# Performance work log

Measured on AMD Instinct MI355X. Metric: run time of the kernel, lower is better.

The kernel has to match this reference:

```python
import jax, jax.numpy as jnp
import numpy as np

C = 256
NUM_HEADS = 8
HEAD_DIM = C // NUM_HEADS
EPS = 1e-5


def setup_inputs() -> dict:
    key = jax.random.key(0)
    ks = jax.random.split(key, 12)
    b, h, w = 8, 64, 64
    s = 1.0 / np.sqrt(C)
    return {
        "cortical": jax.random.normal(ks[0], (b, C, h, w), jnp.float32),
        "subcortical": jax.random.normal(ks[1], (b, C, h, w), jnp.float32),
        "ventricular": jax.random.normal(ks[2], (b, C, h, w), jnp.float32),
        "in_proj_w": jax.random.uniform(ks[3], (3 * C, C), jnp.float32, -s, s),
        "in_proj_b": jnp.zeros((3 * C,), jnp.float32),
        "out_proj_w": jax.random.uniform(ks[4], (C, C), jnp.float32, -s, s),
        "out_proj_b": jnp.zeros((C,), jnp.float32),
        "ln_gamma": jnp.ones((C,), jnp.float32),
        "ln_beta": jnp.zeros((C,), jnp.float32),
        "conv_w": jax.random.uniform(ks[5], (C, 3 * C), jnp.float32, -1.0 / np.sqrt(3 * C), 1.0 / np.sqrt(3 * C)),
        "conv_b": jnp.zeros((C,), jnp.float32),
    }


def _forward(cortical, subcortical, ventricular,
             in_proj_w, in_proj_b, out_proj_w, out_proj_b,
             ln_gamma, ln_beta, conv_w, conv_b):
    b, c, h, w = cortical.shape
    # stack regions -> tokens of seq_len 3: (b,h,w,3,c) -> (N,3,c)
    regions = jnp.stack([cortical, subcortical, ventricular], axis=1)  # (b,3,c,h,w)
    x = regions.transpose(0, 3, 4, 1, 2).reshape(b * h * w, 3, c)
    # fused QKV projection
    qkv = x @ in_proj_w.T + in_proj_b  # (N,3,3c)
    q, k, v = jnp.split(qkv, 3, axis=-1)
    # split heads: (N,3,H,D)
    def heads(t):
        return t.reshape(-1, 3, NUM_HEADS, HEAD_DIM)
    q, k, v = heads(q), heads(k), heads(v)
    scores = jnp.einsum("nshd,nthd->nhst", q, k) / np.sqrt(HEAD_DIM)
    attn = jax.nn.softmax(scores, axis=-1)
    o = jnp.einsum("nhst,nthd->nshd", attn, v).reshape(-1, 3, c)
    o = o @ out_proj_w.T + out_proj_b
    # residual + LayerNorm over channels
    y = o + x
    mu = y.mean(-1, keepdims=True)
    var = y.var(-1, keepdims=True)
    y = (y - mu) * jax.lax.rsqrt(var + EPS) * ln_gamma + ln_beta
    # (N,3,c) -> (b,h,w,3c) region-major == torch cat along channel dim
    fused = y.reshape(b, h, w, 3 * c)
    out = fused @ conv_w.T + conv_b  # 1x1 conv as matmul
    return out.transpose(0, 3, 1, 2)  # (b,c,h,w)


def reference(cortical, subcortical, ventricular, in_proj_w, in_proj_b,
              out_proj_w, out_proj_b, ln_gamma, ln_beta, conv_w, conv_b):
    return _forward(cortical, subcortical, ventricular, in_proj_w, in_proj_b,
                    out_proj_w, out_proj_b, ln_gamma, ln_beta, conv_w, conv_b)
```

## Files before the change

kernel.cpp:

```cpp
#include <hip/hip_runtime.h>

typedef __bf16 bf16x8 __attribute__((ext_vector_type(8)));
typedef float  f32x4  __attribute__((ext_vector_type(4)));

#define XOFF 0
#define OOFF 49152
#define OBUFSZ 7680
#define PSOFF 64512
#define PQOFF 66048
#define MUOFF 67584
#define RSOFF 67968
#define SMEM_BYTES 68352

static __device__ __forceinline__ unsigned short f2b(float f) {
  __bf16 h = (__bf16)f;
  return __builtin_bit_cast(unsigned short, h);
}

__global__ void convert_weights(const float* __restrict__ w_in,
                                const float* __restrict__ w_out,
                                const float* __restrict__ w_conv,
                                __bf16* __restrict__ ws) {
  int gid = blockIdx.x * 256 + threadIdx.x;
  int i4 = gid * 4;
  const float* src;
  int off;
  if (i4 < 196608)      { src = w_in;   off = i4; }
  else if (i4 < 262144) { src = w_out;  off = i4 - 196608; }
  else                  { src = w_conv; off = i4 - 262144; }
  float4 f = *(const float4*)(src + off);
  ws[i4 + 0] = (__bf16)f.x;
  ws[i4 + 1] = (__bf16)f.y;
  ws[i4 + 2] = (__bf16)f.z;
  ws[i4 + 3] = (__bf16)f.w;
}

__global__ __launch_bounds__(256, 2) void crf_fused(
    const float* __restrict__ cort,
    const float* __restrict__ subc,
    const float* __restrict__ vent,
    const __bf16* __restrict__ w_in,
    const float* __restrict__ b_in,
    const __bf16* __restrict__ w_out,
    const float* __restrict__ b_out,
    const float* __restrict__ gamma,
    const float* __restrict__ beta,
    const __bf16* __restrict__ w_conv,
    const float* __restrict__ b_conv,
    float* __restrict__ out) {
  extern __shared__ char smem[];
  const int tid  = threadIdx.x;
  const int lane = tid & 63;
  const int wv   = tid >> 6;
  const int l15  = lane & 15;
  const int l4   = lane >> 4;
  const int blk  = blockIdx.x;
  const int img  = blk >> 7;
  const int pixbase = (blk & 127) << 5;
  const size_t base = (size_t)img * (256 * 4096) + pixbase;

  {
    const float* rp0 = cort + base;
    const float* rp1 = subc + base;
    const float* rp2 = vent + base;
#pragma unroll
    for (int si = 0; si < 3; ++si) {
      const float* rp = (si == 0) ? rp0 : (si == 1) ? rp1 : rp2;
#pragma unroll
      for (int t = 0; t < 16; ++t) {
        int idx = t * 256 + tid;
        int p   = idx & 31;
        int c   = (idx >> 5) * 2;
        float f0 = rp[(size_t)c * 4096 + p];
        float f1 = rp[(size_t)(c + 1) * 4096 + p];
        int m = si * 32 + p;
        unsigned off = ((unsigned)(m * 512 + c * 2)) ^ ((unsigned)(m & 7) << 4);
        unsigned pack = (unsigned)f2b(f0) | ((unsigned)f2b(f1) << 16);
        *(unsigned*)(smem + XOFF + off) = pack;
      }
    }
  }

  f32x4 accY[6][4] = {};

  __syncthreads();

  const int ph = wv & 1;
  const int hg = wv >> 1;
  const float SC = 0.17677669529663687f;

  for (int hh = 0; hh < 4; ++hh) {
    const int h = hg * 4 + hh;
    f32x4 acc[3][6] = {};
#pragma unroll
    for (int ks = 0; ks < 8; ++ks) {
      const int k0 = ks * 32;
      bf16x8 af[3], bfr[6];
#pragma unroll
      for (int s = 0; s < 3; ++s) {
        int m = s * 32 + ph * 16 + l15;
        unsigned off = ((unsigned)(m * 512 + (k0 + l4 * 8) * 2)) ^ ((unsigned)(m & 7) << 4);
        af[s] = *(const bf16x8*)(smem + XOFF + off);
      }
#pragma unroll
      for (int j = 0; j < 6; ++j) {
        int jb = (j >> 1) * 256 + h * 32 + (j & 1) * 16 + l15;
        bfr[j] = *(const bf16x8*)(w_in + (size_t)jb * 256 + k0 + l4 * 8);
      }
#pragma unroll
      for (int s = 0; s < 3; ++s)
#pragma unroll
        for (int j = 0; j < 6; ++j)
          acc[s][j] = __builtin_amdgcn_mfma_f32_16x16x32_bf16(af[s], bfr[j], acc[s][j], 0, 0, 0);
    }
#pragma unroll
    for (int jq = 0; jq < 2; ++jq) {
      float bq = b_in[h * 32 + jq * 16 + l15];
      float bk = b_in[256 + h * 32 + jq * 16 + l15];
      float bv = b_in[512 + h * 32 + jq * 16 + l15];
#pragma unroll
      for (int s = 0; s < 3; ++s)
#pragma unroll
        for (int r = 0; r < 4; ++r) {
          acc[s][jq][r]     += bq;
          acc[s][2 + jq][r] += bk;
          acc[s][4 + jq][r] += bv;
        }
    }
    char* ob = smem + OOFF + hg * OBUFSZ;
#pragma unroll
    for (int si = 0; si < 3; ++si) {
      float pp[3][4];
#pragma unroll
      for (int ti = 0; ti < 3; ++ti)
#pragma unroll
        for (int r = 0; r < 4; ++r)
          pp[ti][r] = acc[si][0][r] * acc[ti][2][r] + acc[si][1][r] * acc[ti][3][r];
#pragma unroll
      for (int mask = 1; mask <= 8; mask <<= 1)
#pragma unroll
        for (int ti = 0; ti < 3; ++ti)
#pragma unroll
          for (int r = 0; r < 4; ++r)
            pp[ti][r] += __shfl_xor(pp[ti][r], mask);
#pragma unroll
      for (int r = 0; r < 4; ++r) {
        float s0 = pp[0][r] * SC, s1 = pp[1][r] * SC, s2 = pp[2][r] * SC;
        float mx = fmaxf(fmaxf(s0, s1), s2);
        float e0 = __expf(s0 - mx), e1 = __expf(s1 - mx), e2 = __expf(s2 - mx);
        float inv = 1.f / (e0 + e1 + e2);
        e0 *= inv; e1 *= inv; e2 *= inv;
        int m = si * 32 + ph * 16 + l4 * 4 + r;
#pragma unroll
        for (int jq = 0; jq < 2; ++jq) {
          float ov = e0 * acc[0][4 + jq][r] + e1 * acc[1][4 + jq][r] + e2 * acc[2][4 + jq][r];
          *(__bf16*)(ob + m * 80 + (jq * 16 + l15) * 2) = (__bf16)ov;
        }
      }
    }
    __syncthreads();

#pragma unroll
    for (int g = 0; g < 2; ++g) {
      const char* obr = smem + OOFF + g * OBUFSZ;
      const int hB = g * 4 + hh;
      bf16x8 af2[6], bf2[4];
#pragma unroll
      for (int i = 0; i < 6; ++i)
        af2[i] = *(const bf16x8*)(obr + (i * 16 + l15) * 80 + l4 * 16);
#pragma unroll
      for (int j = 0; j < 4; ++j) {
        int jr = wv * 64 + j * 16 + l15;
        bf2[j] = *(const bf16x8*)(w_out + (size_t)jr * 256 + hB * 32 + l4 * 8);
      }
#pragma unroll
      for (int i = 0; i < 6; ++i)
#pragma unroll
        for (int j = 0; j < 4; ++j)
          accY[i][j] = __builtin_amdgcn_mfma_f32_16x16x32_bf16(af2[i], bf2[j], accY[i][j], 0, 0, 0);
    }
    __syncthreads();
  }

  float bo[4], gg[4], bb[4];
#pragma unroll
  for (int j = 0; j < 4; ++j) {
    int jc = wv * 64 + j * 16 + l15;
    bo[j] = b_out[jc];
    gg[j] = gamma[jc];
    bb[j] = beta[jc];
  }
#pragma unroll
  for (int i = 0; i < 6; ++i)
#pragma unroll
    for (int r = 0; r < 4; ++r) {
      int m = i * 16 + l4 * 4 + r;
      float s1 = 0.f, s2 = 0.f;
#pragma unroll
      for (int j = 0; j < 4; ++j) {
        int jc = wv * 64 + j * 16 + l15;
        unsigned xo = ((unsigned)(m * 512 + jc * 2)) ^ ((unsigned)(m & 7) << 4);
        float xv = (float)(*(const __bf16*)(smem + XOFF + xo));
        float v = accY[i][j][r] + bo[j] + xv;
        accY[i][j][r] = v;
        s1 += v;
        s2 += v * v;
      }
      s1 += __shfl_xor(s1, 1); s2 += __shfl_xor(s2, 1);
      s1 += __shfl_xor(s1, 2); s2 += __shfl_xor(s2, 2);
      s1 += __shfl_xor(s1, 4); s2 += __shfl_xor(s2, 4);
      s1 += __shfl_xor(s1, 8); s2 += __shfl_xor(s2, 8);
      if (l15 == 0) {
        *(float*)(smem + PSOFF + (m * 4 + wv) * 4) = s1;
        *(float*)(smem + PQOFF + (m * 4 + wv) * 4) = s2;
      }
    }
  __syncthreads();
  if (tid < 96) {
    float s = 0.f, q = 0.f;
#pragma unroll
    for (int j = 0; j < 4; ++j) {
      s += *(const float*)(smem + PSOFF + (tid * 4 + j) * 4);
      q += *(const float*)(smem + PQOFF + (tid * 4 + j) * 4);
    }
    float mu  = s * (1.f / 256.f);
    float var = q * (1.f / 256.f) - mu * mu;
    *(float*)(smem + MUOFF + tid * 4) = mu;
    *(float*)(smem + RSOFF + tid * 4) = rsqrtf(var + 1e-5f);
  }
  __syncthreads();
#pragma unroll
  for (int i = 0; i < 6; ++i)
#pragma unroll
    for (int r = 0; r < 4; ++r) {
      int m = i * 16 + l4 * 4 + r;
      float mu = *(const float*)(smem + MUOFF + m * 4);
      float rs = *(const float*)(smem + RSOFF + m * 4);
      int s = m >> 5, p = m & 31;
#pragma unroll
      for (int j = 0; j < 4; ++j) {
        int jc = wv * 64 + j * 16 + l15;
        float yv = (accY[i][j][r] - mu) * rs * gg[j] + bb[j];
        int kk = s * 256 + jc;
        unsigned off = ((unsigned)(p * 1536 + kk * 2)) ^ ((unsigned)(p & 7) << 4);
        *(__bf16*)(smem + XOFF + off) = (__bf16)yv;
      }
    }
  __syncthreads();

  {
    f32x4 accC[4][2] = {};
#pragma unroll 4
    for (int ks = 0; ks < 24; ++ks) {
      const int k0 = ks * 32;
      bf16x8 af[4], bfr2[2];
#pragma unroll
      for (int i = 0; i < 4; ++i) {
        int co = wv * 64 + i * 16 + l15;
        af[i] = *(const bf16x8*)(w_conv + (size_t)co * 768 + k0 + l4 * 8);
      }
#pragma unroll
      for (int j = 0; j < 2; ++j) {
        int p = j * 16 + l15;
        unsigned off = ((unsigned)(p * 1536 + (k0 + l4 * 8) * 2)) ^ ((unsigned)(p & 7) << 4);
        bfr2[j] = *(const bf16x8*)(smem + XOFF + off);
      }
#pragma unroll
      for (int i = 0; i < 4; ++i)
#pragma unroll
        for (int j = 0; j < 2; ++j)
          accC[i][j] = __builtin_amdgcn_mfma_f32_16x16x32_bf16(af[i], bfr2[j], accC[i][j], 0, 0, 0);
    }
#pragma unroll
    for (int i = 0; i < 4; ++i)
#pragma unroll
      for (int r = 0; r < 4; ++r) {
        int co = wv * 64 + i * 16 + l4 * 4 + r;
        float cb = b_conv[co];
#pragma unroll
        for (int j = 0; j < 2; ++j)
          out[((size_t)img * 256 + co) * 4096 + pixbase + j * 16 + l15] = accC[i][j][r] + cb;
      }
  }
}

extern "C" void kernel_launch(void* const* d_in, const int* in_sizes, int n_in,
                              void* d_out, int out_size, void* d_ws, size_t ws_size,
                              hipStream_t stream) {
  (void)in_sizes; (void)n_in; (void)out_size; (void)ws_size;
  const float* cort    = (const float*)d_in[0];
  const float* subc    = (const float*)d_in[1];
  const float* vent    = (const float*)d_in[2];
  const float* w_in_f  = (const float*)d_in[3];
  const float* b_in    = (const float*)d_in[4];
  const float* w_out_f = (const float*)d_in[5];
  const float* b_out   = (const float*)d_in[6];
  const float* gamma   = (const float*)d_in[7];
  const float* beta    = (const float*)d_in[8];
  const float* w_conv_f= (const float*)d_in[9];
  const float* b_conv  = (const float*)d_in[10];

  __bf16* ws = (__bf16*)d_ws;
  convert_weights<<<448, 256, 0, stream>>>(w_in_f, w_out_f, w_conv_f, ws);
  crf_fused<<<1024, 256, SMEM_BYTES, stream>>>(
      cort, subc, vent,
      ws,            b_in,
      ws + 196608,   b_out,
      gamma,         beta,
      ws + 262144,   b_conv,
      (float*)d_out);
}
```

Measured before the change: 204.4 us.

## Pre-pack bf16 weights into MFMA fragment order for coalesced loads

Weight conversion now writes the bf16 weights in per-lane MFMA fragment order, so each 64-lane wavefront fetches a fragment as one contiguous 1 KB read. Before, each lane read 16 bytes from a different weight row. The fused kernel's in-proj, out-proj and conv weight loads now index this packed layout directly. The aim is fewer memory transactions and better cache-line use for weights re-read from global memory by every block. The pre-pass also launches half as many threads, each converting 8 elements instead of 4.

```diff
diff --git a/kernel.cpp b/kernel.cpp
--- a/kernel.cpp
+++ b/kernel.cpp
@@ -17,22 +17,32 @@
   return __builtin_bit_cast(unsigned short, h);
 }
 
-__global__ void convert_weights(const float* __restrict__ w_in,
-                                const float* __restrict__ w_out,
-                                const float* __restrict__ w_conv,
-                                __bf16* __restrict__ ws) {
-  int gid = blockIdx.x * 256 + threadIdx.x;
-  int i4 = gid * 4;
+__global__ void repack_weights(const float* __restrict__ w_in,
+                               const float* __restrict__ w_out,
+                               const float* __restrict__ w_conv,
+                               __bf16* __restrict__ ws) {
+  int g = blockIdx.x * 256 + threadIdx.x;
+  __bf16* dst = ws + (size_t)g * 8;
   const float* src;
-  int off;
-  if (i4 < 196608)      { src = w_in;   off = i4; }
-  else if (i4 < 262144) { src = w_out;  off = i4 - 196608; }
-  else                  { src = w_conv; off = i4 - 262144; }
-  float4 f = *(const float4*)(src + off);
-  ws[i4 + 0] = (__bf16)f.x;
-  ws[i4 + 1] = (__bf16)f.y;
-  ws[i4 + 2] = (__bf16)f.z;
-  ws[i4 + 3] = (__bf16)f.w;
+  if (g < 24576) {
+    int nt = g >> 9, rem = g & 511;
+    int ks = rem >> 6, lane = rem & 63;
+    src = w_in + (size_t)(nt * 16 + (lane & 15)) * 256 + ks * 32 + (lane >> 4) * 8;
+  } else if (g < 32768) {
+    int g2 = g - 24576;
+    int nt = g2 >> 9, rem = g2 & 511;
+    int ks = rem >> 6, lane = rem & 63;
+    src = w_out + (size_t)(nt * 16 + (lane & 15)) * 256 + ks * 32 + (lane >> 4) * 8;
+  } else {
+    int g3 = g - 32768;
+    int nt = g3 / 1536, rem = g3 - nt * 1536;
+    int ks = rem >> 6, lane = rem & 63;
+    src = w_conv + (size_t)(nt * 16 + (lane & 15)) * 768 + ks * 32 + (lane >> 4) * 8;
+  }
+  float4 a = *(const float4*)src;
+  float4 b = *(const float4*)(src + 4);
+  dst[0]=(__bf16)a.x; dst[1]=(__bf16)a.y; dst[2]=(__bf16)a.z; dst[3]=(__bf16)a.w;
+  dst[4]=(__bf16)b.x; dst[5]=(__bf16)b.y; dst[6]=(__bf16)b.z; dst[7]=(__bf16)b.w;
 }
 
 __global__ __launch_bounds__(256, 2) void crf_fused(
@@ -88,6 +98,9 @@
   const int ph = wv & 1;
   const int hg = wv >> 1;
   const float SC = 0.17677669529663687f;
+  const bf16x8* wif = (const bf16x8*)w_in;
+  const bf16x8* wof = (const bf16x8*)w_out;
+  const bf16x8* wcf = (const bf16x8*)w_conv;
 
   for (int hh = 0; hh < 4; ++hh) {
     const int h = hg * 4 + hh;
@@ -104,8 +117,8 @@
       }
 #pragma unroll
       for (int j = 0; j < 6; ++j) {
-        int jb = (j >> 1) * 256 + h * 32 + (j & 1) * 16 + l15;
-        bfr[j] = *(const bf16x8*)(w_in + (size_t)jb * 256 + k0 + l4 * 8);
+        int nt = (j >> 1) * 16 + h * 2 + (j & 1);
+        bfr[j] = wif[(nt * 8 + ks) * 64 + lane];
       }
 #pragma unroll
       for (int s = 0; s < 3; ++s)
@@ -169,10 +182,8 @@
       for (int i = 0; i < 6; ++i)
         af2[i] = *(const bf16x8*)(obr + (i * 16 + l15) * 80 + l4 * 16);
 #pragma unroll
-      for (int j = 0; j < 4; ++j) {
-        int jr = wv * 64 + j * 16 + l15;
-        bf2[j] = *(const bf16x8*)(w_out + (size_t)jr * 256 + hB * 32 + l4 * 8);
-      }
+      for (int j = 0; j < 4; ++j)
+        bf2[j] = wof[((wv * 4 + j) * 8 + hB) * 64 + lane];
 #pragma unroll
       for (int i = 0; i < 6; ++i)
 #pragma unroll
@@ -182,13 +193,13 @@
     __syncthreads();
   }
 
-  float bo[4], gg[4], bb[4];
+  float bo[4], gg[4], bb2[4];
 #pragma unroll
   for (int j = 0; j < 4; ++j) {
     int jc = wv * 64 + j * 16 + l15;
     bo[j] = b_out[jc];
     gg[j] = gamma[jc];
-    bb[j] = beta[jc];
+    bb2[j] = beta[jc];
   }
 #pragma unroll
   for (int i = 0; i < 6; ++i)
@@ -240,7 +251,7 @@
 #pragma unroll
       for (int j = 0; j < 4; ++j) {
         int jc = wv * 64 + j * 16 + l15;
-        float yv = (accY[i][j][r] - mu) * rs * gg[j] + bb[j];
+        float yv = (accY[i][j][r] - mu) * rs * gg[j] + bb2[j];
         int kk = s * 256 + jc;
         unsigned off = ((unsigned)(p * 1536 + kk * 2)) ^ ((unsigned)(p & 7) << 4);
         *(__bf16*)(smem + XOFF + off) = (__bf16)yv;
@@ -255,10 +266,8 @@
       const int k0 = ks * 32;
       bf16x8 af[4], bfr2[2];
 #pragma unroll
-      for (int i = 0; i < 4; ++i) {
-        int co = wv * 64 + i * 16 + l15;
-        af[i] = *(const bf16x8*)(w_conv + (size_t)co * 768 + k0 + l4 * 8);
-      }
+      for (int i = 0; i < 4; ++i)
+        af[i] = wcf[((wv * 4 + i) * 24 + ks) * 64 + lane];
 #pragma unroll
       for (int j = 0; j < 2; ++j) {
         int p = j * 16 + l15;
@@ -301,7 +310,7 @@
   const float* b_conv  = (const float*)d_in[10];
 
   __bf16* ws = (__bf16*)d_ws;
-  convert_weights<<<448, 256, 0, stream>>>(w_in_f, w_out_f, w_conv_f, ws);
+  repack_weights<<<224, 256, 0, stream>>>(w_in_f, w_out_f, w_conv_f, ws);
   crf_fused<<<1024, 256, SMEM_BYTES, stream>>>(
       cort, subc, vent,
       ws,            b_in,
```

Result: slower. 265.9 us (+30.1%).

## Use 512-thread blocks with one wave per head and single out-proj pass

Applied to the files above, without the earlier changes.

Doubles the block to 8 waves so each wave computes QKV and attention for one full head across all 96 tokens, instead of looping four heads per wave with per-head barriers. The attention output for all heads is written to a swizzled shared buffer, and the out-projection runs as one K=256 GEMM after a single barrier. This removes the per-head synchronisation loop and the split head-group buffers. In exchange, shared memory grows to about 105KB per block and per-wave register pressure rises with the 6x6 accumulator tile, which may limit occupancy.

```diff
diff --git a/kernel.cpp b/kernel.cpp
--- a/kernel.cpp
+++ b/kernel.cpp
@@ -5,12 +5,11 @@
 
 #define XOFF 0
 #define OOFF 49152
-#define OBUFSZ 7680
-#define PSOFF 64512
-#define PQOFF 66048
-#define MUOFF 67584
-#define RSOFF 67968
-#define SMEM_BYTES 68352
+#define PSOFF 98304
+#define PQOFF 101376
+#define MUOFF 104448
+#define RSOFF 104832
+#define SMEM_BYTES 105216
 
 static __device__ __forceinline__ unsigned short f2b(float f) {
   __bf16 h = (__bf16)f;
@@ -35,7 +34,7 @@
   ws[i4 + 3] = (__bf16)f.w;
 }
 
-__global__ __launch_bounds__(256, 2) void crf_fused(
+__global__ __launch_bounds__(512, 2) void crf_fused(
     const float* __restrict__ cort,
     const float* __restrict__ subc,
     const float* __restrict__ vent,
@@ -60,47 +59,38 @@
   const size_t base = (size_t)img * (256 * 4096) + pixbase;
 
   {
-    const float* rp0 = cort + base;
-    const float* rp1 = subc + base;
-    const float* rp2 = vent + base;
 #pragma unroll
     for (int si = 0; si < 3; ++si) {
-      const float* rp = (si == 0) ? rp0 : (si == 1) ? rp1 : rp2;
-#pragma unroll
-      for (int t = 0; t < 16; ++t) {
-        int idx = t * 256 + tid;
+      const float* rp = (si == 0) ? cort : (si == 1) ? subc : vent;
+      rp += base;
+#pragma unroll
+      for (int t = 0; t < 8; ++t) {
+        int idx = t * 512 + tid;
         int p   = idx & 31;
         int c   = (idx >> 5) * 2;
         float f0 = rp[(size_t)c * 4096 + p];
         float f1 = rp[(size_t)(c + 1) * 4096 + p];
         int m = si * 32 + p;
         unsigned off = ((unsigned)(m * 512 + c * 2)) ^ ((unsigned)(m & 7) << 4);
-        unsigned pack = (unsigned)f2b(f0) | ((unsigned)f2b(f1) << 16);
-        *(unsigned*)(smem + XOFF + off) = pack;
-      }
-    }
-  }
-
-  f32x4 accY[6][4] = {};
-
-  __syncthreads();
-
-  const int ph = wv & 1;
-  const int hg = wv >> 1;
-  const float SC = 0.17677669529663687f;
-
-  for (int hh = 0; hh < 4; ++hh) {
-    const int h = hg * 4 + hh;
-    f32x4 acc[3][6] = {};
+        *(unsigned*)(smem + XOFF + off) = (unsigned)f2b(f0) | ((unsigned)f2b(f1) << 16);
+      }
+    }
+  }
+  __syncthreads();
+
+  {
+    const int h = wv;
+    const float SC = 0.17677669529663687f;
+    f32x4 acc[6][6] = {};
 #pragma unroll
     for (int ks = 0; ks < 8; ++ks) {
       const int k0 = ks * 32;
-      bf16x8 af[3], bfr[6];
-#pragma unroll
-      for (int s = 0; s < 3; ++s) {
-        int m = s * 32 + ph * 16 + l15;
+      bf16x8 af[6], bfr[6];
+#pragma unroll
+      for (int mi = 0; mi < 6; ++mi) {
+        int m = mi * 16 + l15;
         unsigned off = ((unsigned)(m * 512 + (k0 + l4 * 8) * 2)) ^ ((unsigned)(m & 7) << 4);
-        af[s] = *(const bf16x8*)(smem + XOFF + off);
+        af[mi] = *(const bf16x8*)(smem + XOFF + off);
       }
 #pragma unroll
       for (int j = 0; j < 6; ++j) {
@@ -108,10 +98,10 @@
         bfr[j] = *(const bf16x8*)(w_in + (size_t)jb * 256 + k0 + l4 * 8);
       }
 #pragma unroll
-      for (int s = 0; s < 3; ++s)
+      for (int mi = 0; mi < 6; ++mi)
 #pragma unroll
         for (int j = 0; j < 6; ++j)
-          acc[s][j] = __builtin_amdgcn_mfma_f32_16x16x32_bf16(af[s], bfr[j], acc[s][j], 0, 0, 0);
+          acc[mi][j] = __builtin_amdgcn_mfma_f32_16x16x32_bf16(af[mi], bfr[j], acc[mi][j], 0, 0, 0);
     }
 #pragma unroll
     for (int jq = 0; jq < 2; ++jq) {
@@ -119,73 +109,80 @@
       float bk = b_in[256 + h * 32 + jq * 16 + l15];
       float bv = b_in[512 + h * 32 + jq * 16 + l15];
 #pragma unroll
-      for (int s = 0; s < 3; ++s)
+      for (int mi = 0; mi < 6; ++mi)
 #pragma unroll
         for (int r = 0; r < 4; ++r) {
-          acc[s][jq][r]     += bq;
-          acc[s][2 + jq][r] += bk;
-          acc[s][4 + jq][r] += bv;
+          acc[mi][jq][r]     += bq;
+          acc[mi][2 + jq][r] += bk;
+          acc[mi][4 + jq][r] += bv;
         }
     }
-    char* ob = smem + OOFF + hg * OBUFSZ;
-#pragma unroll
-    for (int si = 0; si < 3; ++si) {
-      float pp[3][4];
-#pragma unroll
-      for (int ti = 0; ti < 3; ++ti)
-#pragma unroll
-        for (int r = 0; r < 4; ++r)
-          pp[ti][r] = acc[si][0][r] * acc[ti][2][r] + acc[si][1][r] * acc[ti][3][r];
-#pragma unroll
-      for (int mask = 1; mask <= 8; mask <<= 1)
+#pragma unroll
+    for (int pg = 0; pg < 2; ++pg) {
+#pragma unroll
+      for (int si = 0; si < 3; ++si) {
+        float pp[3][4];
 #pragma unroll
         for (int ti = 0; ti < 3; ++ti)
 #pragma unroll
           for (int r = 0; r < 4; ++r)
-            pp[ti][r] += __shfl_xor(pp[ti][r], mask);
-#pragma unroll
-      for (int r = 0; r < 4; ++r) {
-        float s0 = pp[0][r] * SC, s1 = pp[1][r] * SC, s2 = pp[2][r] * SC;
-        float mx = fmaxf(fmaxf(s0, s1), s2);
-        float e0 = __expf(s0 - mx), e1 = __expf(s1 - mx), e2 = __expf(s2 - mx);
-        float inv = 1.f / (e0 + e1 + e2);
-        e0 *= inv; e1 *= inv; e2 *= inv;
-        int m = si * 32 + ph * 16 + l4 * 4 + r;
-#pragma unroll
-        for (int jq = 0; jq < 2; ++jq) {
-          float ov = e0 * acc[0][4 + jq][r] + e1 * acc[1][4 + jq][r] + e2 * acc[2][4 + jq][r];
-          *(__bf16*)(ob + m * 80 + (jq * 16 + l15) * 2) = (__bf16)ov;
+            pp[ti][r] = acc[2 * si + pg][0][r] * acc[2 * ti + pg][2][r]
+                      + acc[2 * si + pg][1][r] * acc[2 * ti + pg][3][r];
+#pragma unroll
+        for (int mask = 1; mask <= 8; mask <<= 1)
+#pragma unroll
+          for (int ti = 0; ti < 3; ++ti)
+#pragma unroll
+            for (int r = 0; r < 4; ++r)
+              pp[ti][r] += __shfl_xor(pp[ti][r], mask);
+#pragma unroll
+        for (int r = 0; r < 4; ++r) {
+          float s0 = pp[0][r] * SC, s1 = pp[1][r] * SC, s2 = pp[2][r] * SC;
+          float mx = fmaxf(fmaxf(s0, s1), s2);
+          float e0 = __expf(s0 - mx), e1 = __expf(s1 - mx), e2 = __expf(s2 - mx);
+          float inv = 1.f / (e0 + e1 + e2);
+          e0 *= inv; e1 *= inv; e2 *= inv;
+          int m = si * 32 + pg * 16 + l4 * 4 + r;
+#pragma unroll
+          for (int jq = 0; jq < 2; ++jq) {
+            float ov = e0 * acc[pg][4 + jq][r] + e1 * acc[2 + pg][4 + jq][r] + e2 * acc[4 + pg][4 + jq][r];
+            int d = h * 32 + jq * 16 + l15;
+            unsigned off = ((unsigned)(m * 512 + d * 2)) ^ ((unsigned)(m & 7) << 4);
+            *(__bf16*)(smem + OOFF + off) = (__bf16)ov;
+          }
         }
       }
     }
-    __syncthreads();
-
-#pragma unroll
-    for (int g = 0; g < 2; ++g) {
-      const char* obr = smem + OOFF + g * OBUFSZ;
-      const int hB = g * 4 + hh;
-      bf16x8 af2[6], bf2[4];
-#pragma unroll
-      for (int i = 0; i < 6; ++i)
-        af2[i] = *(const bf16x8*)(obr + (i * 16 + l15) * 80 + l4 * 16);
-#pragma unroll
-      for (int j = 0; j < 4; ++j) {
-        int jr = wv * 64 + j * 16 + l15;
-        bf2[j] = *(const bf16x8*)(w_out + (size_t)jr * 256 + hB * 32 + l4 * 8);
-      }
-#pragma unroll
-      for (int i = 0; i < 6; ++i)
-#pragma unroll
-        for (int j = 0; j < 4; ++j)
-          accY[i][j] = __builtin_amdgcn_mfma_f32_16x16x32_bf16(af2[i], bf2[j], accY[i][j], 0, 0, 0);
-    }
-    __syncthreads();
-  }
-
-  float bo[4], gg[4], bb[4];
-#pragma unroll
-  for (int j = 0; j < 4; ++j) {
-    int jc = wv * 64 + j * 16 + l15;
+  }
+  __syncthreads();
+
+  f32x4 accY[6][2] = {};
+#pragma unroll
+  for (int ks = 0; ks < 8; ++ks) {
+    const int k0 = ks * 32;
+    bf16x8 af[6], bfr[2];
+#pragma unroll
+    for (int i = 0; i < 6; ++i) {
+      int m = i * 16 + l15;
+      unsigned off = ((unsigned)(m * 512 + (k0 + l4 * 8) * 2)) ^ ((unsigned)(m & 7) << 4);
+      af[i] = *(const bf16x8*)(smem + OOFF + off);
+    }
+#pragma unroll
+    for (int j = 0; j < 2; ++j) {
+      int jr = wv * 32 + j * 16 + l15;
+      bfr[j] = *(const bf16x8*)(w_out + (size_t)jr * 256 + k0 + l4 * 8);
+    }
+#pragma unroll
+    for (int i = 0; i < 6; ++i)
+#pragma unroll
+      for (int j = 0; j < 2; ++j)
+        accY[i][j] = __builtin_amdgcn_mfma_f32_16x16x32_bf16(af[i], bfr[j], accY[i][j], 0, 0, 0);
+  }
+
+  float bo[2], gg[2], bb[2];
+#pragma unroll
+  for (int j = 0; j < 2; ++j) {
+    int jc = wv * 32 + j * 16 + l15;
     bo[j] = b_out[jc];
     gg[j] = gamma[jc];
     bb[j] = beta[jc];
@@ -197,8 +194,8 @@
       int m = i * 16 + l4 * 4 + r;
       float s1 = 0.f, s2 = 0.f;
 #pragma unroll
-      for (int j = 0; j < 4; ++j) {
-        int jc = wv * 64 + j * 16 + l15;
+      for (int j = 0; j < 2; ++j) {
+        int jc = wv * 32 + j * 16 + l15;
         unsigned xo = ((unsigned)(m * 512 + jc * 2)) ^ ((unsigned)(m & 7) << 4);
         float xv = (float)(*(const __bf16*)(smem + XOFF + xo));
         float v = accY[i][j][r] + bo[j] + xv;
@@ -211,17 +208,17 @@
       s1 += __shfl_xor(s1, 4); s2 += __shfl_xor(s2, 4);
       s1 += __shfl_xor(s1, 8); s2 += __shfl_xor(s2, 8);
       if (l15 == 0) {
-        *(float*)(smem + PSOFF + (m * 4 + wv) * 4) = s1;
-        *(float*)(smem + PQOFF + (m * 4 + wv) * 4) = s2;
+        *(float*)(smem + PSOFF + (m * 8 + wv) * 4) = s1;
+        *(float*)(smem + PQOFF + (m * 8 + wv) * 4) = s2;
       }
     }
   __syncthreads();
   if (tid < 96) {
     float s = 0.f, q = 0.f;
 #pragma unroll
-    for (int j = 0; j < 4; ++j) {
-      s += *(const float*)(smem + PSOFF + (tid * 4 + j) * 4);
-      q += *(const float*)(smem + PQOFF + (tid * 4 + j) * 4);
+    for (int j = 0; j < 8; ++j) {
+      s += *(const float*)(smem + PSOFF + (tid * 8 + j) * 4);
+      q += *(const float*)(smem + PQOFF + (tid * 8 + j) * 4);
     }
     float mu  = s * (1.f / 256.f);
     float var = q * (1.f / 256.f) - mu * mu;
@@ -238,8 +235,8 @@
       float rs = *(const float*)(smem + RSOFF + m * 4);
       int s = m >> 5, p = m & 31;
 #pragma unroll
-      for (int j = 0; j < 4; ++j) {
-        int jc = wv * 64 + j * 16 + l15;
+      for (int j = 0; j < 2; ++j) {
+        int jc = wv * 32 + j * 16 + l15;
         float yv = (accY[i][j][r] - mu) * rs * gg[j] + bb[j];
         int kk = s * 256 + jc;
         unsigned off = ((unsigned)(p * 1536 + kk * 2)) ^ ((unsigned)(p & 7) << 4);
@@ -249,14 +246,14 @@
   __syncthreads();
 
   {
-    f32x4 accC[4][2] = {};
+    f32x4 accC[2][2] = {};
 #pragma unroll 4
     for (int ks = 0; ks < 24; ++ks) {
       const int k0 = ks * 32;
-      bf16x8 af[4], bfr2[2];
-#pragma unroll
-      for (int i = 0; i < 4; ++i) {
-        int co = wv * 64 + i * 16 + l15;
+      bf16x8 af[2], bfr2[2];
+#pragma unroll
+      for (int i = 0; i < 2; ++i) {
+        int co = wv * 32 + i * 16 + l15;
         af[i] = *(const bf16x8*)(w_conv + (size_t)co * 768 + k0 + l4 * 8);
       }
 #pragma unroll
@@ -266,16 +263,16 @@
         bfr2[j] = *(const bf16x8*)(smem + XOFF + off);
       }
 #pragma unroll
-      for (int i = 0; i < 4; ++i)
+      for (int i = 0; i < 2; ++i)
 #pragma unroll
         for (int j = 0; j < 2; ++j)
           accC[i][j] = __builtin_amdgcn_mfma_f32_16x16x32_bf16(af[i], bfr2[j], accC[i][j], 0, 0, 0);
     }
 #pragma unroll
-    for (int i = 0; i < 4; ++i)
+    for (int i = 0; i < 2; ++i)
 #pragma unroll
       for (int r = 0; r < 4; ++r) {
-        int co = wv * 64 + i * 16 + l4 * 4 + r;
+        int co = wv * 32 + i * 16 + l4 * 4 + r;
         float cb = b_conv[co];
 #pragma unroll
         for (int j = 0; j < 2; ++j)
@@ -302,7 +299,7 @@
 
   __bf16* ws = (__bf16*)d_ws;
   convert_weights<<<448, 256, 0, stream>>>(w_in_f, w_out_f, w_conv_f, ws);
-  crf_fused<<<1024, 256, SMEM_BYTES, stream>>>(
+  crf_fused<<<1024, 512, SMEM_BYTES, stream>>>(
       cort, subc, vent,
       ws,            b_in,
       ws + 196608,   b_out,
```

Result: slower. 215.2 us (+5.2%).
